# Performance work log

Measured on AMD Instinct MI355X. Metric: run time of the kernel, lower is better.

## Reference

```python
import jax, jax.numpy as jnp
import numpy as np

NUM_FEATURES = 35
BLANK = 2          # local blank index inside each 3-way category
NEG = -1e30        # finite stand-in for -inf (keeps grads NaN-free)


def _ctc_losses(log_probs, ext, skip_ok, valid, input_lengths, target_lengths):
    """Batched CTC negative log-likelihood.
    log_probs: [T,B,F,3] log-softmax per category
    ext:       [B,F,L] extended label sequence (blank interleaved), L=2S+1
    skip_ok:   [B,F,L] whether the l-2 transition is allowed
    valid:     [B,F,L] positions within 2*target_len+1
    Returns per-(B,F) loss.
    """
    T = log_probs.shape[0]

    emit0 = jnp.take_along_axis(log_probs[0], ext, axis=-1)  # [B,F,L]
    alpha = jnp.full_like(emit0, NEG)
    alpha = alpha.at[..., 0].set(emit0[..., 0])
    alpha = alpha.at[..., 1].set(jnp.where(target_lengths > 0, emit0[..., 1], NEG))

    pad1 = jnp.full(alpha.shape[:-1] + (1,), NEG, alpha.dtype)
    pad2 = jnp.full(alpha.shape[:-1] + (2,), NEG, alpha.dtype)

    def step(alpha, xs):
        lp_t, t = xs                                   # lp_t: [B,F,3]
        emit = jnp.take_along_axis(lp_t, ext, axis=-1)  # [B,F,L]
        a1 = jnp.concatenate([pad1, alpha[..., :-1]], axis=-1)
        a2 = jnp.concatenate([pad2, alpha[..., :-2]], axis=-1)
        prev = jnp.logaddexp(jnp.logaddexp(alpha, a1),
                             jnp.where(skip_ok, a2, NEG))
        new = jnp.where(valid, prev + emit, NEG)
        active = (t < input_lengths)[:, None, None]     # [B,1,1]
        return jnp.where(active, new, alpha), None

    alpha, _ = jax.lax.scan(step, alpha, (log_probs[1:], jnp.arange(1, T)))

    idx_last = 2 * target_lengths                       # [B,F] final blank
    last = jnp.take_along_axis(alpha, idx_last[..., None], axis=-1)[..., 0]
    prev_ = jnp.take_along_axis(alpha, jnp.maximum(idx_last - 1, 0)[..., None], axis=-1)[..., 0]
    prev_ = jnp.where(target_lengths > 0, prev_, NEG)
    ll = jnp.logaddexp(last, prev_)
    # zero_infinity=True: impossible alignments contribute 0 loss
    return jnp.where(ll > -1e29, -ll, 0.0)


def reference(logits, targets, input_lengths, target_lengths):
    # logits: [T,B,71]; targets: [B,35,S] local labels in {0,1};
    # input_lengths: [B]; target_lengths: [B,35]
    T, B, _ = logits.shape
    F = NUM_FEATURES
    pos = logits[:, :, :F]
    neg = logits[:, :, F:2 * F]
    blank = jnp.broadcast_to(logits[:, :, 2 * F:2 * F + 1], pos.shape)
    lp = jax.nn.log_softmax(jnp.stack([pos, neg, blank], axis=-1), axis=-1)  # [T,B,F,3]

    S = targets.shape[-1]
    L = 2 * S + 1
    ext = jnp.full((B, F, L), BLANK, jnp.int32).at[:, :, 1::2].set(targets.astype(jnp.int32))
    posL = jnp.arange(L)
    valid = posL[None, None, :] < (2 * target_lengths[..., None] + 1)
    ext_m2 = jnp.pad(ext[:, :, :-2], ((0, 0), (0, 0), (2, 0)), constant_values=BLANK)
    skip_ok = (ext != BLANK) & (ext != ext_m2) & (posL[None, None, :] >= 2)

    loss_bf = _ctc_losses(lp, ext, skip_ok, valid, input_lengths, target_lengths)  # [B,F]
    # reduction='mean': per-sample loss divided by its target length, averaged over batch,
    # then summed over the 35 feature categories (the python loop accumulates per-feature means)
    tl = jnp.maximum(target_lengths, 1).astype(loss_bf.dtype)
    return jnp.sum(jnp.mean(loss_bf / tl, axis=0))


def setup_inputs() -> dict:
    T, B, S = 600, 32, 80
    key = jax.random.key(0)
    k1, k2, k3 = jax.random.split(key, 3)
    logits = jax.random.normal(k1, (T, B, 2 * NUM_FEATURES + 1), dtype=jnp.float32)
    targets = jax.random.randint(k2, (B, NUM_FEATURES, S), 0, 2, dtype=jnp.int32)
    target_lengths = jax.random.randint(k3, (B, NUM_FEATURES), 40, S + 1, dtype=jnp.int32)
    input_lengths = jnp.full((B,), T, dtype=jnp.int32)
    return {"logits": logits, "targets": targets,
            "input_lengths": input_lengths, "target_lengths": target_lengths}
```

## Files before the change

### kernel.cpp

```cpp
#include <hip/hip_runtime.h>

#define LN2 0.6931471805599453f

__device__ __forceinline__ float dpp_shr1_zero(float x) {
    return __int_as_float(__builtin_amdgcn_update_dpp(
        0, __float_as_int(x), 0x138, 0xF, 0xF, true));
}
__device__ __forceinline__ int dpp_shr1_keep(int x) {
    return __builtin_amdgcn_update_dpp(x, x, 0x138, 0xF, 0xF, false);
}
__device__ __forceinline__ float dpp_shl1_zero(float x) {
    return __int_as_float(__builtin_amdgcn_update_dpp(
        0, __float_as_int(x), 0x130, 0xF, 0xF, true));
}
__device__ __forceinline__ int dpp_shl1_keep(int x) {
    return __builtin_amdgcn_update_dpp(x, x, 0x130, 0xF, 0xF, false);
}
__device__ __forceinline__ float exp2i_clamped(int d) {
    int k = 127 + d;
    k = (k < 1) ? 1 : ((k > 254) ? 254 : k);
    return __uint_as_float(((unsigned)k) << 23);
}
__device__ __forceinline__ float sel3(int e, float v0, float v1, float v2) {
    return (e == 2) ? v2 : ((e == 1) ? v1 : v0);
}

struct FwdState {
    float a0, a1, a2;
    float s1, k0, k1;
    int   esum;
};
struct BwdState {
    float c0, c1, c2;
    float s1b, kA, kB;
    int   esum;
};

__device__ __forceinline__ void fwd_step(float em0, float em1, float em2,
                                         FwdState& st, float skm2) {
    float d2 = dpp_shr1_zero(st.a2);
    float d1 = dpp_shr1_zero(st.a1);
    float n0 = fmaf(st.k0, d1, fmaf(st.s1, d2, st.a0)) * em0;
    float n1 = fmaf(st.k1, d2, st.a1 + st.a0) * em1;
    float n2 = fmaf(skm2, st.a0, st.a2 + st.a1) * em2;
    st.a0 = n0; st.a1 = n1; st.a2 = n2;
}
__device__ __forceinline__ void bwd_step(float em0, float em1, float em2,
                                         BwdState& st, float skm2) {
    float d3 = dpp_shl1_zero(st.c0);
    float d4 = dpp_shl1_zero(st.c1);
    float n0 = fmaf(skm2, st.c2, st.c0 + st.c1) * em0;
    float n1 = fmaf(st.kA, d3, st.c1 + st.c2) * em1;
    float n2 = fmaf(st.kB, d4, fmaf(st.s1b, d3, st.c2)) * em2;
    st.c0 = n0; st.c1 = n1; st.c2 = n2;
}

__device__ __forceinline__ void fwd_rescale(FwdState& st, float skm0, float skm1) {
    float m = fmaxf(fmaxf(st.a0, st.a1), st.a2);
    int ebits = (int)(__float_as_uint(m) >> 23);
    bool dead = (ebits == 0);
    int de = dead ? 0 : (127 - ebits);
    float scz = dead ? 0.0f : exp2i_clamped(de);
    st.a0 *= scz; st.a1 *= scz; st.a2 *= scz;
    st.esum -= de;
    #pragma unroll
    for (int r = 0; r < 5; ++r) {
        int en = dpp_shr1_keep(st.esum);
        st.esum = dead ? en : st.esum;
    }
    int enf = dpp_shr1_keep(st.esum);
    int gap = enf - st.esum;
    int adj = (gap > 64) ? (gap - 64) : 0;
    float sc3 = exp2i_clamped(-adj);
    st.a0 *= sc3; st.a1 *= sc3; st.a2 *= sc3;
    st.esum += adj;
    st.s1 = exp2i_clamped(gap - adj);
    st.k0 = skm0 * st.s1;
    st.k1 = skm1 * st.s1;
}
__device__ __forceinline__ void bwd_rescale(BwdState& st, float sknA, float sknB) {
    float m = fmaxf(fmaxf(st.c0, st.c1), st.c2);
    int ebits = (int)(__float_as_uint(m) >> 23);
    bool dead = (ebits == 0);
    int de = dead ? 0 : (127 - ebits);
    float scz = dead ? 0.0f : exp2i_clamped(de);
    st.c0 *= scz; st.c1 *= scz; st.c2 *= scz;
    st.esum -= de;
    #pragma unroll
    for (int r = 0; r < 5; ++r) {
        int en = dpp_shl1_keep(st.esum);
        st.esum = dead ? en : st.esum;
    }
    #pragma unroll
    for (int r = 0; r < 3; ++r) {
        int enl = dpp_shr1_keep(st.esum);
        int mn = (enl < st.esum) ? enl : st.esum;
        st.esum = dead ? mn : st.esum;
    }
    int deadR = dpp_shl1_keep(dead ? 1 : 0);
    int enf = dpp_shl1_keep(st.esum);
    int gap = enf - st.esum;
    int adj = (gap > 64) ? (gap - 64) : 0;
    adj = (adj > 126) ? 126 : adj;
    adj = deadR ? 0 : adj;
    float sc3 = exp2i_clamped(-adj);
    st.c0 *= sc3; st.c1 *= sc3; st.c2 *= sc3;
    st.esum += adj;
    float s1b = exp2i_clamped(gap - adj);
    st.s1b = deadR ? 0.f : s1b;
    st.kA = sknA * st.s1b;
    st.kB = sknB * st.s1b;
}

__global__ __launch_bounds__(64, 1) void ctc_kernel(
    const float* __restrict__ logits,
    const int* __restrict__ targets,
    const int* __restrict__ input_lengths,
    const int* __restrict__ target_lengths,
    float* __restrict__ loss_out,
    int T, int B, int Ff, int S)
{
    const int p = blockIdx.x;
    const int b = p / Ff;
    const int f = p - b * Ff;
    const int lane = (int)threadIdx.x;
    const int C = 2 * Ff + 1;
    const int L = 2 * S + 1;

    const int tl = target_lengths[p];
    const int il = input_lengths[b];
    const int tbase = p * S;

    int e0i, e1i, e2i;
    float skm0, skm1, skm2;
    {
        int e[3]; float sk[3];
        const int l0 = 3 * lane;
        #pragma unroll
        for (int j = 0; j < 3; ++j) {
            int l = l0 + j;
            int ev = 2; float sok = 0.f;
            if (l < L && (l & 1)) {
                int s = (l - 1) >> 1;
                ev = targets[tbase + s];
                if (s >= 1) sok = (targets[tbase + s - 1] != ev) ? 1.f : 0.f;
            }
            e[j] = ev; sk[j] = sok;
        }
        e0i = e[0]; e1i = e[1]; e2i = e[2];
        skm0 = sk[0]; skm1 = sk[1]; skm2 = sk[2];
    }
    const float sknA = dpp_shl1_zero(skm0);
    const float sknB = dpp_shl1_zero(skm1);

    __shared__ float4 slp[608];
    {
        const float* lg = logits + (size_t)b * C;
        const size_t strideT = (size_t)B * C;
        float c0 = 0.f, c1 = 0.f, c2 = 0.f;
        if (lane < T) {
            const float* r = lg + (size_t)lane * strideT;
            c0 = r[f]; c1 = r[Ff + f]; c2 = r[2 * Ff];
        }
        #pragma unroll 1
        for (int j = 0; j < 10; ++j) {
            int i = lane + (j << 6);
            int inx = i + 64;
            float n0 = 0.f, n1 = 0.f, n2 = 0.f;
            if (inx < T) {
                const float* r = lg + (size_t)inx * strideT;
                n0 = r[f]; n1 = r[Ff + f]; n2 = r[2 * Ff];
            }
            float4 v = make_float4(0.f, 0.f, 0.f, 0.f);
            if (i < T) {
                float m = fmaxf(fmaxf(c0, c1), c2);
                float ep = __expf(c0 - m);
                float en = __expf(c1 - m);
                float eb = __expf(c2 - m);
                float inv = __builtin_amdgcn_rcpf(ep + en + eb);
                v = make_float4(ep * inv, en * inv, eb * inv, 0.f);
            }
            if (i < 608) slp[i] = v;
            c0 = n0; c1 = n1; c2 = n2;
        }
    }
    __syncthreads();

    const char* base8 = (const char*)slp;
    const char* qt0 = base8 + (e0i << 2);
    const char* qt1 = base8 + (e1i << 2);
    const char* qt2 = base8 + (e2i << 2);

    const int TL = (il < T) ? il : T;
    const int m_ = (TL >= 2) ? ((TL - 1) >> 1) : 0;
    const int Bk = (TL >= 2) ? (TL - 2 - m_) : 0;
    const int F  = m_;
    const int P  = (F < Bk) ? F : Bk;
    const int nblk = P >> 3;

    FwdState fs;
    BwdState bs;
    {
        float4 E0 = slp[0];
        fs.a0 = (lane == 0) ? E0.z : 0.f;
        fs.a1 = (lane == 0 && tl > 0) ? sel3(e1i, E0.x, E0.y, E0.z) : 0.f;
        fs.a2 = 0.f;
        fs.s1 = 1.f; fs.k0 = skm0; fs.k1 = skm1;
        fs.esum = 0;

        int oTL = (TL - 1) << 4;
        float eL0 = *(const float*)(qt0 + oTL);
        float eL1 = *(const float*)(qt1 + oTL);
        float eL2 = *(const float*)(qt2 + oTL);
        int l0i = 3 * lane;
        int end1 = 2 * tl, end2 = 2 * tl - 1;
        bs.c0 = (l0i == end1 || l0i == end2) ? eL0 : 0.f;
        bs.c1 = (l0i + 1 == end1 || l0i + 1 == end2) ? eL1 : 0.f;
        bs.c2 = (l0i + 2 == end1 || l0i + 2 == end2) ? eL2 : 0.f;
        bs.s1b = 1.f; bs.kA = sknA; bs.kB = sknB;
        bs.esum = 0;
    }

    const char* pf0 = qt0 + 16;
    const char* pf1 = qt1 + 16;
    const char* pf2 = qt2 + 16;
    const char* pb0 = qt0 + ((TL - 2) << 4);
    const char* pb1 = qt1 + ((TL - 2) << 4);
    const char* pb2 = qt2 + ((TL - 2) << 4);
#define LDF(OFF, E) { E[0] = *(const float*)(pf0 + (OFF)); \
                      E[1] = *(const float*)(pf1 + (OFF)); \
                      E[2] = *(const float*)(pf2 + (OFF)); }
#define LDB(OFF, E) { E[0] = *(const float*)(pb0 - (OFF)); \
                      E[1] = *(const float*)(pb1 - (OFF)); \
                      E[2] = *(const float*)(pb2 - (OFF)); }
    float FA0[3], FA1[3], FA2[3], FA3[3], FB0[3], FB1[3], FB2[3], FB3[3];
    float GA0[3], GA1[3], GA2[3], GA3[3], GB0[3], GB1[3], GB2[3], GB3[3];
    if (nblk > 0) {
        LDF(  0, FA0); LDF( 16, FA1); LDF( 32, FA2); LDF( 48, FA3);
        LDF( 64, FB0); LDF( 80, FB1); LDF( 96, FB2); LDF(112, FB3);
        LDB(  0, GA0); LDB( 16, GA1); LDB( 32, GA2); LDB( 48, GA3);
        LDB( 64, GB0); LDB( 80, GB1); LDB( 96, GB2); LDB(112, GB3);
    }
    for (int blk = 0; blk < nblk; ++blk) {
        fwd_rescale(fs, skm0, skm1);
        bwd_rescale(bs, sknA, sknB);
        fwd_step(FA0[0], FA0[1], FA0[2], fs, skm2);
        bwd_step(GA0[0], GA0[1], GA0[2], bs, skm2);
        fwd_step(FA1[0], FA1[1], FA1[2], fs, skm2);
        bwd_step(GA1[0], GA1[1], GA1[2], bs, skm2);
        fwd_step(FA2[0], FA2[1], FA2[2], fs, skm2);
        bwd_step(GA2[0], GA2[1], GA2[2], bs, skm2);
        fwd_step(FA3[0], FA3[1], FA3[2], fs, skm2);
        bwd_step(GA3[0], GA3[1], GA3[2], bs, skm2);
        LDF(128, FA0); LDF(144, FA1); LDF(160, FA2); LDF(176, FA3);
        LDB(128, GA0); LDB(144, GA1); LDB(160, GA2); LDB(176, GA3);
        fwd_step(FB0[0], FB0[1], FB0[2], fs, skm2);
        bwd_step(GB0[0], GB0[1], GB0[2], bs, skm2);
        fwd_step(FB1[0], FB1[1], FB1[2], fs, skm2);
        bwd_step(GB1[0], GB1[1], GB1[2], bs, skm2);
        fwd_step(FB2[0], FB2[1], FB2[2], fs, skm2);
        bwd_step(GB2[0], GB2[1], GB2[2], bs, skm2);
        fwd_step(FB3[0], FB3[1], FB3[2], fs, skm2);
        bwd_step(GB3[0], GB3[1], GB3[2], bs, skm2);
        LDF(192, FB0); LDF(208, FB1); LDF(224, FB2); LDF(240, FB3);
        LDB(192, GB0); LDB(208, GB1); LDB(224, GB2); LDB(240, GB3);
        pf0 += 128; pf1 += 128; pf2 += 128;
        pb0 -= 128; pb1 -= 128; pb2 -= 128;
    }
#undef LDF
#undef LDB
    int tf = 8 * nblk + 1;
    int tb = TL - 2 - 8 * nblk;
    while (tf <= F && tb >= m_ + 1) {
        int of = tf << 4, ob = tb << 4;
        float f0 = *(const float*)(qt0 + of);
        float f1 = *(const float*)(qt1 + of);
        float f2 = *(const float*)(qt2 + of);
        float g0 = *(const float*)(qt0 + ob);
        float g1 = *(const float*)(qt1 + ob);
        float g2 = *(const float*)(qt2 + ob);
        fwd_step(f0, f1, f2, fs, skm2);
        bwd_step(g0, g1, g2, bs, skm2);
        ++tf; --tb;
    }
    while (tf <= F) {
        int of = tf << 4;
        float f0 = *(const float*)(qt0 + of);
        float f1 = *(const float*)(qt1 + of);
        float f2 = *(const float*)(qt2 + of);
        fwd_step(f0, f1, f2, fs, skm2);
        ++tf;
    }
    while (tb >= m_ + 1) {
        int ob = tb << 4;
        float g0 = *(const float*)(qt0 + ob);
        float g1 = *(const float*)(qt1 + ob);
        float g2 = *(const float*)(qt2 + ob);
        bwd_step(g0, g1, g2, bs, skm2);
        --tb;
    }

    __shared__ float sa[192];
    __shared__ float sg[194];
    __shared__ int   seb[65];
    __shared__ float sdot[64];
    __shared__ int   sE[64];
    {
        int l0b = 3 * lane;
        sa[l0b] = fs.a0; sa[l0b + 1] = fs.a1; sa[l0b + 2] = fs.a2;
        sg[l0b] = bs.c0; sg[l0b + 1] = bs.c1; sg[l0b + 2] = bs.c2;
        seb[lane] = bs.esum;
        if (lane == 0) { sg[192] = 0.f; sg[193] = 0.f; seb[64] = 0; }
    }
    __syncthreads();
    {
        float scn = exp2i_clamped(seb[lane + 1] - bs.esum);
        float g3 = sg[3 * lane + 3] * scn;
        float g4 = sg[3 * lane + 4] * scn;
        float s0 = fmaf(skm2, bs.c2, bs.c0 + bs.c1);
        float s1 = fmaf(sknA, g3, bs.c1 + bs.c2);
        float s2 = fmaf(sknB, g4, bs.c2 + g3);
        float dot = fs.a0 * s0 + fs.a1 * s1 + fs.a2 * s2;
        sdot[lane] = dot;
        sE[lane] = fs.esum + bs.esum;
    }
    __syncthreads();
    if (lane == 0) {
        float loss = 0.f;
        if (TL == 1) {
            float v = sa[2 * tl] + ((tl > 0) ? sa[2 * tl - 1] : 0.f);
            if (v > 0.f) loss = -(__log2f(v) * LN2);
        } else {
            int Emax = -0x40000000;
            for (int i = 0; i < 64; ++i)
                if (sdot[i] > 0.f && sE[i] > Emax) Emax = sE[i];
            if (Emax != -0x40000000) {
                float sum = 0.f;
                for (int i = 0; i < 64; ++i) {
                    int d = sE[i] - Emax;
                    if (d > -127 && sdot[i] > 0.f) sum += sdot[i] * exp2i_clamped(d);
                }
                loss = -((__log2f(sum) + (float)Emax) * LN2);
            }
        }
        float denom = (tl > 0) ? (float)tl : 1.0f;
        loss_out[p] = loss / denom;
    }
}

__global__ __launch_bounds__(256) void reduce_kernel(
    const float* __restrict__ v, float* __restrict__ out, int n, float invB)
{
    __shared__ float buf[256];
    float s = 0.f;
    for (int i = (int)threadIdx.x; i < n; i += 256) s += v[i];
    buf[threadIdx.x] = s;
    __syncthreads();
    for (int off = 128; off > 0; off >>= 1) {
        if ((int)threadIdx.x < off) buf[threadIdx.x] += buf[threadIdx.x + off];
        __syncthreads();
    }
    if (threadIdx.x == 0) out[0] = buf[0] * invB;
}

extern "C" void kernel_launch(void* const* d_in, const int* in_sizes, int n_in,
                              void* d_out, int out_size, void* d_ws, size_t ws_size,
                              hipStream_t stream) {
    const float* logits         = (const float*)d_in[0];
    const int*   targets        = (const int*)d_in[1];
    const int*   input_lengths  = (const int*)d_in[2];
    const int*   target_lengths = (const int*)d_in[3];
    float* out = (float*)d_out;

    const int B  = in_sizes[2];
    const int BF = in_sizes[3];
    const int Ff = BF / B;
    const int S  = in_sizes[1] / BF;
    const int C  = 2 * Ff + 1;
    const int T  = in_sizes[0] / (B * C);

    float* losses = (float*)d_ws;

    ctc_kernel<<<BF, 64, 0, stream>>>(logits, targets, input_lengths,
                                      target_lengths, losses, T, B, Ff, S);
    reduce_kernel<<<1, 256, 0, stream>>>(losses, out, BF, 1.0f / (float)B);
}
```

Before: 64.80 us.

## Split forward and backward CTC recursions across two wavefronts per block

Each block now has two wavefronts. Wave 0 runs the forward alpha recursion and wave 1 runs the backward recursion, where before one wave interleaved both. The logit softmax preload is spread over 128 threads, and each recursion loop unrolls 16 steps with a rescale every 8. This shortens the serial dependency chain per wave, since the two recursions can now issue on separate SIMDs. In exchange it doubles the threads per block and leans on the scheduler placing the two waves on different SIMDs, which 1120 blocks may not always allow.

Measured after the change: 53.01 us. 18.2% less time.

```diff
diff --git a/kernel.cpp b/kernel.cpp
--- a/kernel.cpp
+++ b/kernel.cpp
@@ -1,6 +1,8 @@
 #include <hip/hip_runtime.h>
 
 #define LN2 0.6931471805599453f
+
+typedef float f32x4 __attribute__((ext_vector_type(4)));
 
 __device__ __forceinline__ float dpp_shr1_zero(float x) {
     return __int_as_float(__builtin_amdgcn_update_dpp(
@@ -112,7 +114,7 @@
     st.kB = sknB * st.s1b;
 }
 
-__global__ __launch_bounds__(64, 1) void ctc_kernel(
+__global__ __launch_bounds__(128, 1) void ctc_kernel(
     const float* __restrict__ logits,
     const int* __restrict__ targets,
     const int* __restrict__ input_lengths,
@@ -123,7 +125,9 @@
     const int p = blockIdx.x;
     const int b = p / Ff;
     const int f = p - b * Ff;
-    const int lane = (int)threadIdx.x;
+    const int tid = (int)threadIdx.x;
+    const int wid = tid >> 6;
+    const int lane = tid & 63;
     const int C = 2 * Ff + 1;
     const int L = 2 * S + 1;
 
@@ -153,34 +157,34 @@
     const float sknA = dpp_shl1_zero(skm0);
     const float sknB = dpp_shl1_zero(skm1);
 
-    __shared__ float4 slp[608];
+    __shared__ f32x4 slp[640];
     {
         const float* lg = logits + (size_t)b * C;
         const size_t strideT = (size_t)B * C;
         float c0 = 0.f, c1 = 0.f, c2 = 0.f;
-        if (lane < T) {
-            const float* r = lg + (size_t)lane * strideT;
+        if (tid < T) {
+            const float* r = lg + (size_t)tid * strideT;
             c0 = r[f]; c1 = r[Ff + f]; c2 = r[2 * Ff];
         }
         #pragma unroll 1
-        for (int j = 0; j < 10; ++j) {
-            int i = lane + (j << 6);
-            int inx = i + 64;
+        for (int j = 0; j < 5; ++j) {
+            int i = tid + (j << 7);
+            int inx = i + 128;
             float n0 = 0.f, n1 = 0.f, n2 = 0.f;
             if (inx < T) {
                 const float* r = lg + (size_t)inx * strideT;
                 n0 = r[f]; n1 = r[Ff + f]; n2 = r[2 * Ff];
             }
-            float4 v = make_float4(0.f, 0.f, 0.f, 0.f);
+            f32x4 v = {0.f, 0.f, 0.f, 0.f};
             if (i < T) {
                 float m = fmaxf(fmaxf(c0, c1), c2);
                 float ep = __expf(c0 - m);
                 float en = __expf(c1 - m);
                 float eb = __expf(c2 - m);
                 float inv = __builtin_amdgcn_rcpf(ep + en + eb);
-                v = make_float4(ep * inv, en * inv, eb * inv, 0.f);
+                v[0] = ep * inv; v[1] = en * inv; v[2] = eb * inv;
             }
-            if (i < 608) slp[i] = v;
+            if (i < 640) slp[i] = v;
             c0 = n0; c1 = n1; c2 = n2;
         }
     }
@@ -193,139 +197,171 @@
 
     const int TL = (il < T) ? il : T;
     const int m_ = (TL >= 2) ? ((TL - 1) >> 1) : 0;
+    const int Fn = m_;
     const int Bk = (TL >= 2) ? (TL - 2 - m_) : 0;
-    const int F  = m_;
-    const int P  = (F < Bk) ? F : Bk;
-    const int nblk = P >> 3;
-
-    FwdState fs;
-    BwdState bs;
-    {
-        float4 E0 = slp[0];
-        fs.a0 = (lane == 0) ? E0.z : 0.f;
-        fs.a1 = (lane == 0 && tl > 0) ? sel3(e1i, E0.x, E0.y, E0.z) : 0.f;
-        fs.a2 = 0.f;
-        fs.s1 = 1.f; fs.k0 = skm0; fs.k1 = skm1;
-        fs.esum = 0;
-
-        int oTL = (TL - 1) << 4;
-        float eL0 = *(const float*)(qt0 + oTL);
-        float eL1 = *(const float*)(qt1 + oTL);
-        float eL2 = *(const float*)(qt2 + oTL);
-        int l0i = 3 * lane;
-        int end1 = 2 * tl, end2 = 2 * tl - 1;
-        bs.c0 = (l0i == end1 || l0i == end2) ? eL0 : 0.f;
-        bs.c1 = (l0i + 1 == end1 || l0i + 1 == end2) ? eL1 : 0.f;
-        bs.c2 = (l0i + 2 == end1 || l0i + 2 == end2) ? eL2 : 0.f;
-        bs.s1b = 1.f; bs.kA = sknA; bs.kB = sknB;
-        bs.esum = 0;
-    }
-
-    const char* pf0 = qt0 + 16;
-    const char* pf1 = qt1 + 16;
-    const char* pf2 = qt2 + 16;
-    const char* pb0 = qt0 + ((TL - 2) << 4);
-    const char* pb1 = qt1 + ((TL - 2) << 4);
-    const char* pb2 = qt2 + ((TL - 2) << 4);
-#define LDF(OFF, E) { E[0] = *(const float*)(pf0 + (OFF)); \
-                      E[1] = *(const float*)(pf1 + (OFF)); \
-                      E[2] = *(const float*)(pf2 + (OFF)); }
-#define LDB(OFF, E) { E[0] = *(const float*)(pb0 - (OFF)); \
-                      E[1] = *(const float*)(pb1 - (OFF)); \
-                      E[2] = *(const float*)(pb2 - (OFF)); }
-    float FA0[3], FA1[3], FA2[3], FA3[3], FB0[3], FB1[3], FB2[3], FB3[3];
-    float GA0[3], GA1[3], GA2[3], GA3[3], GB0[3], GB1[3], GB2[3], GB3[3];
-    if (nblk > 0) {
-        LDF(  0, FA0); LDF( 16, FA1); LDF( 32, FA2); LDF( 48, FA3);
-        LDF( 64, FB0); LDF( 80, FB1); LDF( 96, FB2); LDF(112, FB3);
-        LDB(  0, GA0); LDB( 16, GA1); LDB( 32, GA2); LDB( 48, GA3);
-        LDB( 64, GB0); LDB( 80, GB1); LDB( 96, GB2); LDB(112, GB3);
-    }
-    for (int blk = 0; blk < nblk; ++blk) {
-        fwd_rescale(fs, skm0, skm1);
-        bwd_rescale(bs, sknA, sknB);
-        fwd_step(FA0[0], FA0[1], FA0[2], fs, skm2);
-        bwd_step(GA0[0], GA0[1], GA0[2], bs, skm2);
-        fwd_step(FA1[0], FA1[1], FA1[2], fs, skm2);
-        bwd_step(GA1[0], GA1[1], GA1[2], bs, skm2);
-        fwd_step(FA2[0], FA2[1], FA2[2], fs, skm2);
-        bwd_step(GA2[0], GA2[1], GA2[2], bs, skm2);
-        fwd_step(FA3[0], FA3[1], FA3[2], fs, skm2);
-        bwd_step(GA3[0], GA3[1], GA3[2], bs, skm2);
-        LDF(128, FA0); LDF(144, FA1); LDF(160, FA2); LDF(176, FA3);
-        LDB(128, GA0); LDB(144, GA1); LDB(160, GA2); LDB(176, GA3);
-        fwd_step(FB0[0], FB0[1], FB0[2], fs, skm2);
-        bwd_step(GB0[0], GB0[1], GB0[2], bs, skm2);
-        fwd_step(FB1[0], FB1[1], FB1[2], fs, skm2);
-        bwd_step(GB1[0], GB1[1], GB1[2], bs, skm2);
-        fwd_step(FB2[0], FB2[1], FB2[2], fs, skm2);
-        bwd_step(GB2[0], GB2[1], GB2[2], bs, skm2);
-        fwd_step(FB3[0], FB3[1], FB3[2], fs, skm2);
-        bwd_step(GB3[0], GB3[1], GB3[2], bs, skm2);
-        LDF(192, FB0); LDF(208, FB1); LDF(224, FB2); LDF(240, FB3);
-        LDB(192, GB0); LDB(208, GB1); LDB(224, GB2); LDB(240, GB3);
-        pf0 += 128; pf1 += 128; pf2 += 128;
-        pb0 -= 128; pb1 -= 128; pb2 -= 128;
-    }
-#undef LDF
-#undef LDB
-    int tf = 8 * nblk + 1;
-    int tb = TL - 2 - 8 * nblk;
-    while (tf <= F && tb >= m_ + 1) {
-        int of = tf << 4, ob = tb << 4;
-        float f0 = *(const float*)(qt0 + of);
-        float f1 = *(const float*)(qt1 + of);
-        float f2 = *(const float*)(qt2 + of);
-        float g0 = *(const float*)(qt0 + ob);
-        float g1 = *(const float*)(qt1 + ob);
-        float g2 = *(const float*)(qt2 + ob);
-        fwd_step(f0, f1, f2, fs, skm2);
-        bwd_step(g0, g1, g2, bs, skm2);
-        ++tf; --tb;
-    }
-    while (tf <= F) {
-        int of = tf << 4;
-        float f0 = *(const float*)(qt0 + of);
-        float f1 = *(const float*)(qt1 + of);
-        float f2 = *(const float*)(qt2 + of);
-        fwd_step(f0, f1, f2, fs, skm2);
-        ++tf;
-    }
-    while (tb >= m_ + 1) {
-        int ob = tb << 4;
-        float g0 = *(const float*)(qt0 + ob);
-        float g1 = *(const float*)(qt1 + ob);
-        float g2 = *(const float*)(qt2 + ob);
-        bwd_step(g0, g1, g2, bs, skm2);
-        --tb;
-    }
 
     __shared__ float sa[192];
     __shared__ float sg[194];
     __shared__ int   seb[65];
     __shared__ float sdot[64];
     __shared__ int   sE[64];
-    {
-        int l0b = 3 * lane;
-        sa[l0b] = fs.a0; sa[l0b + 1] = fs.a1; sa[l0b + 2] = fs.a2;
-        sg[l0b] = bs.c0; sg[l0b + 1] = bs.c1; sg[l0b + 2] = bs.c2;
-        seb[lane] = bs.esum;
-        if (lane == 0) { sg[192] = 0.f; sg[193] = 0.f; seb[64] = 0; }
+
+    FwdState fs;
+    fs.a0 = 0.f; fs.a1 = 0.f; fs.a2 = 0.f; fs.s1 = 1.f;
+    fs.k0 = skm0; fs.k1 = skm1; fs.esum = 0;
+
+    if (wid == 0) {
+        {
+            f32x4 E0 = slp[0];
+            fs.a0 = (lane == 0) ? E0[2] : 0.f;
+            fs.a1 = (lane == 0 && tl > 0) ? sel3(e1i, E0[0], E0[1], E0[2]) : 0.f;
+            fs.a2 = 0.f;
+        }
+        const int t_endF = Fn + 1;
+        const char* pr0 = qt0 + 16;
+        const char* pr1 = qt1 + 16;
+        const char* pr2 = qt2 + 16;
+#define LDE(OFF, E) { E[0] = *(const float*)(pr0 + (OFF)); \
+                      E[1] = *(const float*)(pr1 + (OFF)); \
+                      E[2] = *(const float*)(pr2 + (OFF)); }
+        float A0[3], A1[3], A2[3], A3[3], B0[3], B1[3], B2[3], B3[3];
+        float C0[3], C1[3], C2[3], C3[3], D0[3], D1[3], D2[3], D3[3];
+        int t = 1;
+        if (t + 15 < t_endF) {
+            LDE(  0, A0); LDE( 16, A1); LDE( 32, A2); LDE( 48, A3);
+            LDE( 64, B0); LDE( 80, B1); LDE( 96, B2); LDE(112, B3);
+            LDE(128, C0); LDE(144, C1); LDE(160, C2); LDE(176, C3);
+            LDE(192, D0); LDE(208, D1); LDE(224, D2); LDE(240, D3);
+        }
+        #pragma unroll 1
+        for (; t + 15 < t_endF; t += 16) {
+            fwd_rescale(fs, skm0, skm1);
+            fwd_step(A0[0], A0[1], A0[2], fs, skm2);
+            fwd_step(A1[0], A1[1], A1[2], fs, skm2);
+            fwd_step(A2[0], A2[1], A2[2], fs, skm2);
+            fwd_step(A3[0], A3[1], A3[2], fs, skm2);
+            LDE(256, A0); LDE(272, A1); LDE(288, A2); LDE(304, A3);
+            fwd_step(B0[0], B0[1], B0[2], fs, skm2);
+            fwd_step(B1[0], B1[1], B1[2], fs, skm2);
+            fwd_step(B2[0], B2[1], B2[2], fs, skm2);
+            fwd_step(B3[0], B3[1], B3[2], fs, skm2);
+            LDE(320, B0); LDE(336, B1); LDE(352, B2); LDE(368, B3);
+            fwd_rescale(fs, skm0, skm1);
+            fwd_step(C0[0], C0[1], C0[2], fs, skm2);
+            fwd_step(C1[0], C1[1], C1[2], fs, skm2);
+            fwd_step(C2[0], C2[1], C2[2], fs, skm2);
+            fwd_step(C3[0], C3[1], C3[2], fs, skm2);
+            LDE(384, C0); LDE(400, C1); LDE(416, C2); LDE(432, C3);
+            fwd_step(D0[0], D0[1], D0[2], fs, skm2);
+            fwd_step(D1[0], D1[1], D1[2], fs, skm2);
+            fwd_step(D2[0], D2[1], D2[2], fs, skm2);
+            fwd_step(D3[0], D3[1], D3[2], fs, skm2);
+            LDE(448, D0); LDE(464, D1); LDE(480, D2); LDE(496, D3);
+            pr0 += 256; pr1 += 256; pr2 += 256;
+        }
+#undef LDE
+        #pragma unroll 1
+        for (; t < t_endF; ++t) {
+            int o = t << 4;
+            float e0 = *(const float*)(qt0 + o);
+            float e1 = *(const float*)(qt1 + o);
+            float e2 = *(const float*)(qt2 + o);
+            fwd_step(e0, e1, e2, fs, skm2);
+        }
+        {
+            int l = 3 * lane;
+            sa[l] = fs.a0; sa[l + 1] = fs.a1; sa[l + 2] = fs.a2;
+        }
+    } else {
+        BwdState bs;
+        {
+            int oTL = (TL - 1) << 4;
+            float eL0 = *(const float*)(qt0 + oTL);
+            float eL1 = *(const float*)(qt1 + oTL);
+            float eL2 = *(const float*)(qt2 + oTL);
+            int l0i = 3 * lane;
+            int end1 = 2 * tl, end2 = 2 * tl - 1;
+            bs.c0 = (l0i == end1 || l0i == end2) ? eL0 : 0.f;
+            bs.c1 = (l0i + 1 == end1 || l0i + 1 == end2) ? eL1 : 0.f;
+            bs.c2 = (l0i + 2 == end1 || l0i + 2 == end2) ? eL2 : 0.f;
+            bs.s1b = 1.f; bs.kA = sknA; bs.kB = sknB;
+            bs.esum = 0;
+        }
+        const char* pb0 = qt0 + ((TL - 2) << 4);
+        const char* pb1 = qt1 + ((TL - 2) << 4);
+        const char* pb2 = qt2 + ((TL - 2) << 4);
+#define LDB(OFF, E) { E[0] = *(const float*)(pb0 - (OFF)); \
+                      E[1] = *(const float*)(pb1 - (OFF)); \
+                      E[2] = *(const float*)(pb2 - (OFF)); }
+        float GA0[3], GA1[3], GA2[3], GA3[3], GB0[3], GB1[3], GB2[3], GB3[3];
+        float GC0[3], GC1[3], GC2[3], GC3[3], GD0[3], GD1[3], GD2[3], GD3[3];
+        int k = 0;
+        if (k + 15 < Bk) {
+            LDB(  0, GA0); LDB( 16, GA1); LDB( 32, GA2); LDB( 48, GA3);
+            LDB( 64, GB0); LDB( 80, GB1); LDB( 96, GB2); LDB(112, GB3);
+            LDB(128, GC0); LDB(144, GC1); LDB(160, GC2); LDB(176, GC3);
+            LDB(192, GD0); LDB(208, GD1); LDB(224, GD2); LDB(240, GD3);
+        }
+        #pragma unroll 1
+        for (; k + 15 < Bk; k += 16) {
+            bwd_rescale(bs, sknA, sknB);
+            bwd_step(GA0[0], GA0[1], GA0[2], bs, skm2);
+            bwd_step(GA1[0], GA1[1], GA1[2], bs, skm2);
+            bwd_step(GA2[0], GA2[1], GA2[2], bs, skm2);
+            bwd_step(GA3[0], GA3[1], GA3[2], bs, skm2);
+            LDB(256, GA0); LDB(272, GA1); LDB(288, GA2); LDB(304, GA3);
+            bwd_step(GB0[0], GB0[1], GB0[2], bs, skm2);
+            bwd_step(GB1[0], GB1[1], GB1[2], bs, skm2);
+            bwd_step(GB2[0], GB2[1], GB2[2], bs, skm2);
+            bwd_step(GB3[0], GB3[1], GB3[2], bs, skm2);
+            LDB(320, GB0); LDB(336, GB1); LDB(352, GB2); LDB(368, GB3);
+            bwd_rescale(bs, sknA, sknB);
+            bwd_step(GC0[0], GC0[1], GC0[2], bs, skm2);
+            bwd_step(GC1[0], GC1[1], GC1[2], bs, skm2);
+            bwd_step(GC2[0], GC2[1], GC2[2], bs, skm2);
+            bwd_step(GC3[0], GC3[1], GC3[2], bs, skm2);
+            LDB(384, GC0); LDB(400, GC1); LDB(416, GC2); LDB(432, GC3);
+            bwd_step(GD0[0], GD0[1], GD0[2], bs, skm2);
+            bwd_step(GD1[0], GD1[1], GD1[2], bs, skm2);
+            bwd_step(GD2[0], GD2[1], GD2[2], bs, skm2);
+            bwd_step(GD3[0], GD3[1], GD3[2], bs, skm2);
+            LDB(448, GD0); LDB(464, GD1); LDB(480, GD2); LDB(496, GD3);
+            pb0 -= 256; pb1 -= 256; pb2 -= 256;
+        }
+#undef LDB
+        int trow = TL - 2 - k;
+        #pragma unroll 1
+        for (; trow >= m_ + 1; --trow) {
+            int o = trow << 4;
+            float g0 = *(const float*)(qt0 + o);
+            float g1 = *(const float*)(qt1 + o);
+            float g2 = *(const float*)(qt2 + o);
+            bwd_step(g0, g1, g2, bs, skm2);
+        }
+        {
+            int l = 3 * lane;
+            sg[l] = bs.c0; sg[l + 1] = bs.c1; sg[l + 2] = bs.c2;
+            seb[lane] = bs.esum;
+            if (lane == 0) { sg[192] = 0.f; sg[193] = 0.f; seb[64] = 0; }
+        }
     }
     __syncthreads();
-    {
-        float scn = exp2i_clamped(seb[lane + 1] - bs.esum);
+
+    if (wid == 0) {
+        int eB = seb[lane];
+        float scn = exp2i_clamped(seb[lane + 1] - eB);
+        float g0 = sg[3 * lane], g1 = sg[3 * lane + 1], g2 = sg[3 * lane + 2];
         float g3 = sg[3 * lane + 3] * scn;
         float g4 = sg[3 * lane + 4] * scn;
-        float s0 = fmaf(skm2, bs.c2, bs.c0 + bs.c1);
-        float s1 = fmaf(sknA, g3, bs.c1 + bs.c2);
-        float s2 = fmaf(sknB, g4, bs.c2 + g3);
+        float s0 = fmaf(skm2, g2, g0 + g1);
+        float s1 = fmaf(sknA, g3, g1 + g2);
+        float s2 = fmaf(sknB, g4, g2 + g3);
         float dot = fs.a0 * s0 + fs.a1 * s1 + fs.a2 * s2;
         sdot[lane] = dot;
-        sE[lane] = fs.esum + bs.esum;
+        sE[lane] = fs.esum + eB;
     }
     __syncthreads();
-    if (lane == 0) {
+    if (tid == 0) {
         float loss = 0.f;
         if (TL == 1) {
             float v = sa[2 * tl] + ((tl > 0) ? sa[2 * tl - 1] : 0.f);
@@ -381,7 +417,7 @@
 
     float* losses = (float*)d_ws;
 
-    ctc_kernel<<<BF, 64, 0, stream>>>(logits, targets, input_lengths,
-                                      target_lengths, losses, T, B, Ff, S);
+    ctc_kernel<<<BF, 128, 0, stream>>>(logits, targets, input_lengths,
+                                       target_lengths, losses, T, B, Ff, S);
     reduce_kernel<<<1, 256, 0, stream>>>(losses, out, BF, 1.0f / (float)B);
 }
```
